# Optimization experiments

Hardware: AMD Instinct MI355X
Metric: run time of the kernel (lower is better)

Reference implementation:

```python
import jax, jax.numpy as jnp
import numpy as np

N_TOKENS = 16384
D_IN = 1024
D_HID = 4096
D_OUT = 1024
N_EXPERTS = 8


def setup_inputs() -> dict:
    key = jax.random.key(0)
    ks = jax.random.split(key, 7)
    s_in = 1.0 / np.sqrt(D_IN)
    s_hid = 1.0 / np.sqrt(D_HID)
    return {
        "x": jax.random.normal(ks[0], (N_TOKENS, D_IN), dtype=jnp.float32),
        "Wr": jax.random.uniform(ks[1], (D_IN, N_EXPERTS), jnp.float32, -s_in, s_in),
        "br": jax.random.uniform(ks[2], (N_EXPERTS,), jnp.float32, -s_in, s_in),
        "W1": jax.random.uniform(ks[3], (N_EXPERTS, D_IN, D_HID), jnp.float32, -s_in, s_in),
        "b1": jax.random.uniform(ks[4], (N_EXPERTS, D_HID), jnp.float32, -s_in, s_in),
        "W2": jax.random.uniform(ks[5], (N_EXPERTS, D_HID, D_OUT), jnp.float32, -s_hid, s_hid),
        "b2": jax.random.uniform(ks[6], (N_EXPERTS, D_OUT), jnp.float32, -s_hid, s_hid),
    }


def reference(x, Wr, br, W1, b1, W2, b2):
    # Router: softmax over expert logits, hard top-1 dispatch (argmax).
    # Note: output is NOT scaled by routing probs in the original module.
    logits = x @ Wr + br                      # [N, E]
    expert_idx = jnp.argmax(logits, axis=-1)  # [N] (argmax of softmax == argmax of logits)

    n_experts = W1.shape[0]
    out = jnp.zeros((x.shape[0], W2.shape[-1]), dtype=x.dtype)
    # world_size=1 -> all_to_all is identity; masked per-expert dense FFN + combine.
    # Fixed small loop over experts (structurally distinct weights), vectorized over tokens.
    for e in range(n_experts):
        mask = (expert_idx == e)[:, None]                 # [N, 1]
        xe = jnp.where(mask, x, 0.0)                      # zero out tokens not routed here
        y = jax.nn.relu(xe @ W1[e] + b1[e]) @ W2[e] + b2[e]  # [N, D_OUT]
        out = jnp.where(mask, y, out)
    return out
```

## Files before the change

kernel.cpp:

```cpp
#include <hip/hip_runtime.h>
#include <cstdint>

#define NT   16384
#define DIN  1024
#define DHID 4096
#define DOUT 1024
#define NE   8
#define NMT  136
#define NMT2 72

typedef unsigned short u16;
typedef short bf16x8 __attribute__((ext_vector_type(8)));
typedef float f32x4  __attribute__((ext_vector_type(4)));

__device__ __forceinline__ u16 f2b(float f) {
  union { float f; unsigned u; } a; a.f = f;
  unsigned u = a.u;
  return (u16)((u + 0x7FFFu + ((u >> 16) & 1u)) >> 16);
}

__device__ __forceinline__ void gl_lds16(const u16* g, u16* l) {
  __builtin_amdgcn_global_load_lds(
      (const __attribute__((address_space(1))) void*)g,
      (__attribute__((address_space(3))) void*)l,
      16, 0, 0);
}

__device__ __forceinline__ void barrier_raw() {
  asm volatile("" ::: "memory");
  __builtin_amdgcn_s_barrier();
  asm volatile("" ::: "memory");
}
__device__ __forceinline__ void lgkm0() {
  asm volatile("s_waitcnt lgkmcnt(0)" ::: "memory");
  __builtin_amdgcn_sched_barrier(0);
}
__device__ __forceinline__ void vm6() {
  asm volatile("s_waitcnt vmcnt(6)" ::: "memory");
}

__global__ void router_kernel(const float* __restrict__ x, const float* __restrict__ Wr,
                              const float* __restrict__ br, u16* __restrict__ Xb,
                              int* __restrict__ eidx, int* __restrict__ counts) {
  int t = blockIdx.x * 4 + (threadIdx.x >> 6);
  int lane = threadIdx.x & 63;
  const float4* xr = (const float4*)(x + (size_t)t * DIN);
  ushort4* xbr = (ushort4*)(Xb + (size_t)t * DIN);
  float acc[NE];
#pragma unroll
  for (int e = 0; e < NE; e++) acc[e] = 0.f;
#pragma unroll
  for (int i = 0; i < DIN / 256; i++) {
    int q = lane + i * 64;
    float4 xv = xr[q];
    ushort4 o;
    o.x = f2b(xv.x); o.y = f2b(xv.y); o.z = f2b(xv.z); o.w = f2b(xv.w);
    xbr[q] = o;
    const float* wp = Wr + (size_t)q * 4 * NE;
#pragma unroll
    for (int kk = 0; kk < 4; kk++) {
      float xs = (&xv.x)[kk];
      const float4 w0 = *(const float4*)(wp + kk * NE);
      const float4 w1 = *(const float4*)(wp + kk * NE + 4);
      acc[0] += xs * w0.x; acc[1] += xs * w0.y; acc[2] += xs * w0.z; acc[3] += xs * w0.w;
      acc[4] += xs * w1.x; acc[5] += xs * w1.y; acc[6] += xs * w1.z; acc[7] += xs * w1.w;
    }
  }
#pragma unroll
  for (int off = 32; off > 0; off >>= 1) {
#pragma unroll
    for (int e = 0; e < NE; e++) acc[e] += __shfl_down(acc[e], off, 64);
  }
  if (lane == 0) {
    int best = 0; float bv = acc[0] + br[0];
#pragma unroll
    for (int e = 1; e < NE; e++) {
      float v = acc[e] + br[e];
      if (v > bv) { bv = v; best = e; }
    }
    eidx[t] = best;
    atomicAdd(&counts[best], 1);
  }
}

__global__ void zero_kernel(int* __restrict__ p) {
  if (threadIdx.x < 16) p[threadIdx.x] = 0;
}

__global__ void scan_kernel(const int* __restrict__ counts, int* __restrict__ offsets,
                            int4* __restrict__ tiles, int4* __restrict__ tiles2) {
  if (threadIdx.x == 0) {
    int s = 0, nt = 0, nt2 = 0;
    for (int e = 0; e < NE; e++) {
      int c = counts[e];
      offsets[e] = s;
      for (int m0 = 0; m0 < c; m0 += 128) {
        int v = c - m0; if (v > 128) v = 128;
        tiles[nt++] = make_int4(e, s + m0, v, 0);
      }
      for (int m0 = 0; m0 < c; m0 += 256) {
        int v = c - m0; if (v > 256) v = 256;
        tiles2[nt2++] = make_int4(e, s + m0, v, 0);
      }
      s += c;
    }
    offsets[NE] = s;
    while (nt < NMT) tiles[nt++] = make_int4(0, 0, 0, 0);
    while (nt2 < NMT2) tiles2[nt2++] = make_int4(0, 0, 0, 0);
  }
}

__global__ void scatter_kernel(const int* __restrict__ eidx, const int* __restrict__ offsets,
                               int* __restrict__ cursor, int* __restrict__ perm) {
  int t = blockIdx.x * blockDim.x + threadIdx.x;
  if (t >= NT) return;
  int e = eidx[t];
  int pos = offsets[e] + atomicAdd(&cursor[e], 1);
  perm[pos] = t;
}

__global__ void transpose_cvt_all(const float* __restrict__ W1, const float* __restrict__ W2,
                                  u16* __restrict__ W1t, u16* __restrict__ W2t) {
  __shared__ float tile[64][65];
  int bid = blockIdx.x;
  const float* src; u16* dst; int K, H, k0, h0;
  if (bid < NE * 16 * 64) {
    int e = bid >> 10, rem = bid & 1023;
    K = DIN; H = DHID;
    k0 = (rem & 15) * 64; h0 = (rem >> 4) * 64;
    src = W1 + (size_t)e * DIN * DHID; dst = W1t + (size_t)e * DIN * DHID;
  } else {
    bid -= NE * 16 * 64;
    int e = bid >> 10, rem = bid & 1023;
    K = DHID; H = DOUT;
    k0 = (rem >> 4) * 64; h0 = (rem & 15) * 64;
    src = W2 + (size_t)e * DHID * DOUT; dst = W2t + (size_t)e * DHID * DOUT;
  }
  const int tid = threadIdx.x;
#pragma unroll
  for (int i = 0; i < 4; i++) {
    int idx = tid + i * 256;
    int r = idx >> 4;
    int c = (idx & 15) * 4;
    const float4 v = *(const float4*)(src + (size_t)(k0 + r) * H + h0 + c);
    tile[r][c] = v.x; tile[r][c + 1] = v.y; tile[r][c + 2] = v.z; tile[r][c + 3] = v.w;
  }
  __syncthreads();
#pragma unroll
  for (int i = 0; i < 4; i++) {
    int idx = tid + i * 256;
    int r = idx >> 4;
    int c = (idx & 15) * 4;
    ushort4 o;
    o.x = f2b(tile[c][r]); o.y = f2b(tile[c + 1][r]);
    o.z = f2b(tile[c + 2][r]); o.w = f2b(tile[c + 3][r]);
    *(ushort4*)(dst + (size_t)(h0 + r) * K + k0 + c) = o;
  }
}

template<bool GATHER_A, bool STORE_HIDDEN>
__global__ __launch_bounds__(256) void moe_gemm(
    const u16* __restrict__ A, const u16* __restrict__ Bt,
    const float* __restrict__ bias,
    const int* __restrict__ perm, const int4* __restrict__ tiles,
    u16* __restrict__ Hout, float* __restrict__ Fout,
    int K, int N) {
  const int4 ti = tiles[blockIdx.y];
  const int valid = ti.z;
  if (valid == 0) return;
  const int e = ti.x;
  const int base_p = ti.y;
  const int n0 = blockIdx.x * 128;

  __shared__ u16 sA[2 * 128 * 32];
  __shared__ u16 sB[2 * 128 * 32];

  const int tid = threadIdx.x;
  const int lane = tid & 63;
  const int wave = tid >> 6;
  const int wm = (wave >> 1) * 64;
  const int wn = (wave & 1) * 64;
  const int quad = lane >> 4;
  const int l15 = lane & 15;

  const int rr = lane >> 2;
  const int cb = (lane & 3) * 8;

  const int rA0 = wave * 16 + rr;
  const int rA1 = rA0 + 64;

  int pa0 = base_p + rA0; if (pa0 > NT - 1) pa0 = NT - 1;
  int pa1 = base_p + rA1; if (pa1 > NT - 1) pa1 = NT - 1;
  const int arow0 = GATHER_A ? perm[pa0] : pa0;
  const int arow1 = GATHER_A ? perm[pa1] : pa1;
  const u16* aptr0 = A + (size_t)arow0 * K + cb;
  const u16* aptr1 = A + (size_t)arow1 * K + cb;
  const u16* bptr0 = Bt + ((size_t)e * N + n0 + rA0) * K + cb;
  const u16* bptr1 = Bt + ((size_t)e * N + n0 + rA1) * K + cb;

  u16* dA0 = &sA[wave * 512];
  u16* dA1 = &sA[wave * 512 + 2048];
  u16* dB0 = &sB[wave * 512];
  u16* dB1 = &sB[wave * 512 + 2048];

  f32x4 acc[4][4];
#pragma unroll
  for (int mi = 0; mi < 4; mi++)
#pragma unroll
    for (int ni = 0; ni < 4; ni++)
      acc[mi][ni] = (f32x4){0.f, 0.f, 0.f, 0.f};

  const int kiters = K >> 6;
  for (int kt = 0; kt < kiters; kt++) {
    if (kt) __syncthreads();
    gl_lds16(aptr0,      dA0);
    gl_lds16(aptr1,      dA1);
    gl_lds16(bptr0,      dB0);
    gl_lds16(bptr1,      dB1);
    gl_lds16(aptr0 + 32, dA0 + 4096);
    gl_lds16(aptr1 + 32, dA1 + 4096);
    gl_lds16(bptr0 + 32, dB0 + 4096);
    gl_lds16(bptr1 + 32, dB1 + 4096);
    aptr0 += 64; aptr1 += 64; bptr0 += 64; bptr1 += 64;
    __syncthreads();

#pragma unroll
    for (int h = 0; h < 2; h++) {
      bf16x8 af[4], bfr[4];
#pragma unroll
      for (int mi = 0; mi < 4; mi++)
        af[mi] = *(const bf16x8*)&sA[h * 4096 + (wm + mi * 16 + l15) * 32 + quad * 8];
#pragma unroll
      for (int ni = 0; ni < 4; ni++)
        bfr[ni] = *(const bf16x8*)&sB[h * 4096 + (wn + ni * 16 + l15) * 32 + quad * 8];
#pragma unroll
      for (int mi = 0; mi < 4; mi++)
#pragma unroll
        for (int ni = 0; ni < 4; ni++)
          acc[mi][ni] = __builtin_amdgcn_mfma_f32_16x16x32_bf16(af[mi], bfr[ni], acc[mi][ni], 0, 0, 0);
    }
  }

  float bv[4];
#pragma unroll
  for (int ni = 0; ni < 4; ni++)
    bv[ni] = bias[(size_t)e * N + n0 + wn + ni * 16 + l15];

#pragma unroll
  for (int mi = 0; mi < 4; mi++) {
#pragma unroll
    for (int r = 0; r < 4; r++) {
      const int ml = wm + mi * 16 + quad * 4 + r;
      if (ml >= valid) continue;
      const int pp = base_p + ml;
      if (STORE_HIDDEN) {
        u16* orow = Hout + (size_t)pp * N + n0 + wn;
#pragma unroll
        for (int ni = 0; ni < 4; ni++) {
          float v = acc[mi][ni][r] + bv[ni];
          v = v > 0.f ? v : 0.f;
          orow[ni * 16 + l15] = f2b(v);
        }
      } else {
        const int token = perm[pp];
        float* orow = Fout + (size_t)token * N + n0 + wn;
#pragma unroll
        for (int ni = 0; ni < 4; ni++)
          orow[ni * 16 + l15] = acc[mi][ni][r] + bv[ni];
      }
    }
  }
}

#define RXA0 0
#define RXA1 8192
#define RXB0 16384
#define RXB1 24576
#define RYA0 32768
#define RYA1 40960
#define RYB0 49152
#define RYB1 57344

__global__ __launch_bounds__(512, 2) void moe_gemm1_8ph(
    const u16* __restrict__ A, const u16* __restrict__ Bt,
    const float* __restrict__ bias, const int* __restrict__ perm,
    const int4* __restrict__ tiles, u16* __restrict__ Hout) {
  const int4 ti = tiles[blockIdx.y];
  const int valid = ti.z;
  if (valid == 0) return;
  const int e = ti.x;
  const int base_p = ti.y;
  const int n0 = blockIdx.x * 256;

  __shared__ u16 lds[65536];

  const int tid = threadIdx.x;
  const int lane = tid & 63;
  const int w = tid >> 6;
  const int wr = w >> 2;
  const int wc = w & 3;
  const int quad = lane >> 4;
  const int l15 = lane & 15;

  const int srow = tid >> 3;
  const int klog = ((tid & 7) << 3) ^ ((srow & 7) << 3);
  int p0 = base_p + srow;        if (p0 > NT - 1) p0 = NT - 1;
  int p1 = base_p + 64 + srow;   if (p1 > NT - 1) p1 = NT - 1;
  int p2 = base_p + 128 + srow;  if (p2 > NT - 1) p2 = NT - 1;
  int p3 = base_p + 192 + srow;  if (p3 > NT - 1) p3 = NT - 1;
  const u16* pA00 = A + (size_t)perm[p0] * DIN + klog;
  const u16* pA01 = A + (size_t)perm[p1] * DIN + klog;
  const u16* pA10 = A + (size_t)perm[p2] * DIN + klog;
  const u16* pA11 = A + (size_t)perm[p3] * DIN + klog;
  const u16* pB00 = Bt + ((size_t)e * DHID + n0 + srow)       * DIN + klog;
  const u16* pB01 = Bt + ((size_t)e * DHID + n0 + 64 + srow)  * DIN + klog;
  const u16* pB10 = Bt + ((size_t)e * DHID + n0 + 128 + srow) * DIN + klog;
  const u16* pB11 = Bt + ((size_t)e * DHID + n0 + 192 + srow) * DIN + klog;

#define STG(RB, P0, P1, KO) \
  do { gl_lds16((P0) + (KO), &lds[(RB) + w * 512]); \
       gl_lds16((P1) + (KO), &lds[(RB) + 4096 + w * 512]); } while (0)

  STG(RXA0, pA00, pA01, 0);
  STG(RXA1, pA10, pA11, 0);
  STG(RXB0, pB00, pB01, 0);
  STG(RXB1, pB10, pB11, 0);
  STG(RYB0, pB00, pB01, 64);
  STG(RYB1, pB10, pB11, 64);
  STG(RYA0, pA00, pA01, 64);
  vm6();
  barrier_raw();

  const int aX = RXA0 + wr * 8192;
  const int bX = RXB0 + (wc >> 1) * 8192;
  const int aY = RYA0 + wr * 8192;
  const int bY = RYB0 + (wc >> 1) * 8192;
  const int swz = (l15 & 7) << 3;
  const int brow = (wc & 1) * 64 + l15;

  bf16x8 aF[4][2], bF[4][2];
  f32x4 acc[8][4];
#pragma unroll
  for (int i = 0; i < 8; i++)
#pragma unroll
    for (int j2 = 0; j2 < 4; j2++) acc[i][j2] = (f32x4){0.f, 0.f, 0.f, 0.f};

#define RDA(BASE, MH) do { _Pragma("unroll") \
  for (int mi = 0; mi < 4; mi++) { _Pragma("unroll") \
    for (int h = 0; h < 2; h++) \
      aF[mi][h] = *(const bf16x8*)&lds[(BASE) + ((MH) * 64 + mi * 16 + l15) * 64 + \
                                       ((h * 32 + quad * 8) ^ swz)]; } } while (0)

#define RDB(BASE) do { _Pragma("unroll") \
  for (int ni = 0; ni < 4; ni++) { _Pragma("unroll") \
    for (int h = 0; h < 2; h++) \
      bF[ni][h] = *(const bf16x8*)&lds[(BASE) + (brow + ni * 16) * 64 + \
                                       ((h * 32 + quad * 8) ^ swz)]; } } while (0)

#define MM(MH, NB) do { __builtin_amdgcn_s_setprio(1); _Pragma("unroll") \
  for (int mi = 0; mi < 4; mi++) { _Pragma("unroll") \
    for (int ni = 0; ni < 2; ni++) { _Pragma("unroll") \
      for (int h = 0; h < 2; h++) \
        acc[(MH) * 4 + mi][(NB) + ni] = __builtin_amdgcn_mfma_f32_16x16x32_bf16( \
            aF[mi][h], bF[(NB) + ni][h], acc[(MH) * 4 + mi][(NB) + ni], 0, 0, 0); } } \
  __builtin_amdgcn_s_setprio(0); } while (0)

  const int NITER = DIN / 128;
  for (int j = 0; j < NITER; j++) {
    const int ky1 = (2 * j + 1) * 64;
    int t2 = 2 * j + 2; if (t2 > 15) t2 = 15;
    int t3 = 2 * j + 3; if (t3 > 15) t3 = 15;
    const int kx = t2 * 64, ky2 = t3 * 64;
    RDA(aX, 0); RDB(bX);
    STG(RYA1, pA10, pA11, ky1);
    barrier_raw(); lgkm0();
    MM(0, 0);
    barrier_raw();
    STG(RXB0, pB00, pB01, kx);
    barrier_raw(); lgkm0();
    MM(0, 2);
    barrier_raw();
    RDA(aX, 1);
    STG(RXB1, pB10, pB11, kx);
    barrier_raw(); lgkm0();
    MM(1, 2);
    barrier_raw();
    STG(RXA0, pA00, pA01, kx);
    barrier_raw(); lgkm0();
    MM(1, 0);
    vm6();
    barrier_raw();
    RDA(aY, 0); RDB(bY);
    STG(RXA1, pA10, pA11, kx);
    barrier_raw(); lgkm0();
    MM(0, 0);
    barrier_raw();
    STG(RYB0, pB00, pB01, ky2);
    barrier_raw(); lgkm0();
    MM(0, 2);
    barrier_raw();
    RDA(aY, 1);
    STG(RYB1, pB10, pB11, ky2);
    barrier_raw(); lgkm0();
    MM(1, 2);
    barrier_raw();
    STG(RYA0, pA00, pA01, ky2);
    barrier_raw(); lgkm0();
    MM(1, 0);
    vm6();
    barrier_raw();
  }

  const int col0 = n0 + wc * 64;
  float bv[4];
#pragma unroll
  for (int ni = 0; ni < 4; ni++)
    bv[ni] = bias[(size_t)e * DHID + col0 + ni * 16 + l15];
#pragma unroll
  for (int mi8 = 0; mi8 < 8; mi8++) {
#pragma unroll
    for (int r = 0; r < 4; r++) {
      const int ml = wr * 128 + mi8 * 16 + quad * 4 + r;
      if (ml >= valid) continue;
      u16* orow = Hout + (size_t)(base_p + ml) * DHID + col0;
#pragma unroll
      for (int ni = 0; ni < 4; ni++) {
        float v = acc[mi8][ni][r] + bv[ni];
        v = v > 0.f ? v : 0.f;
        orow[ni * 16 + l15] = f2b(v);
      }
    }
  }
#undef STG
#undef RDA
#undef RDB
#undef MM
}

__global__ void sentinel_kernel(float* __restrict__ out, int n) {
  int i = blockIdx.x * blockDim.x + threadIdx.x;
  if (i < n) out[i] = 31337.0f;
}

extern "C" void kernel_launch(void* const* d_in, const int* in_sizes, int n_in,
                              void* d_out, int out_size, void* d_ws, size_t ws_size,
                              hipStream_t stream) {
  const float* x  = (const float*)d_in[0];
  const float* Wr = (const float*)d_in[1];
  const float* br = (const float*)d_in[2];
  const float* W1 = (const float*)d_in[3];
  const float* b1 = (const float*)d_in[4];
  const float* W2 = (const float*)d_in[5];
  const float* b2 = (const float*)d_in[6];
  float* out = (float*)d_out;

  const size_t szXb  = (size_t)NT * DIN * 2;
  const size_t szW1t = (size_t)NE * DIN * DHID * 2;
  const size_t szW2t = (size_t)NE * DHID * DOUT * 2;
  const size_t szHid = (size_t)NT * DHID * 2;
  char* ws = (char*)d_ws;
  u16* Xb   = (u16*)ws;
  u16* W1t  = (u16*)(ws + szXb);
  u16* W2t  = (u16*)(ws + szXb + szW1t);
  u16* Hid  = (u16*)(ws + szXb + szW1t + szW2t);
  int* perm = (int*)(ws + szXb + szW1t + szW2t + szHid);
  int* eidx = perm + NT;
  int* ctrl = eidx + NT;
  int* counts  = ctrl;
  int* cursor  = ctrl + 8;
  int* offsets = ctrl + 16;
  int4* tiles   = (int4*)(ctrl + 32);
  int4* tiles2  = tiles + NMT;
  const size_t NEED = szXb + szW1t + szW2t + szHid + (size_t)NT * 4 * 2 + 4096;

  if (ws_size < NEED) {
    sentinel_kernel<<<(out_size + 255) / 256, 256, 0, stream>>>(out, out_size);
    return;
  }

  zero_kernel<<<1, 64, 0, stream>>>(ctrl);
  transpose_cvt_all<<<NE * 16 * 64 * 2, 256, 0, stream>>>(W1, W2, W1t, W2t);
  router_kernel<<<NT / 4, 256, 0, stream>>>(x, Wr, br, Xb, eidx, counts);
  scan_kernel<<<1, 64, 0, stream>>>(counts, offsets, tiles, tiles2);
  scatter_kernel<<<NT / 256, 256, 0, stream>>>(eidx, offsets, cursor, perm);

  moe_gemm1_8ph<<<dim3(DHID / 256, NMT2), 512, 0, stream>>>(
      Xb, W1t, b1, perm, tiles2, Hid);
  moe_gemm<false, false><<<dim3(DOUT / 128, NMT), 256, 0, stream>>>(
      Hid, W2t, b2, perm, tiles, nullptr, out, DHID, DOUT);
}
```

Baseline: 1.016 ms.

## Remap MoE GEMM grids to 1D swizzled order and skip MFMA for empty wave rows

Both grouped GEMMs now use a 1D grid whose block index is remapped so that consecutive blocks cover different tiles across groups (g*17+j, g*9+j), spreading expert tiles across XCDs for better L2 reuse. Waves whose row range lies entirely beyond the valid row count of a partially filled tile skip LDS fragment reads and MFMA work, but still take part in staging and barriers. In the first GEMM the B-fragment read is also split into two halves so the second half is loaded just before it is used, which lowers register pressure. The cost is extra branching around the MFMA blocks and a fixed coupling of the remap to NMT/NMT2 sizes.

After: 991.2 us. 1.03x faster.

```diff
diff --git a/kernel.cpp b/kernel.cpp
--- a/kernel.cpp
+++ b/kernel.cpp
@@ -158,19 +158,24 @@
   }
 }
 
-template<bool GATHER_A, bool STORE_HIDDEN>
-__global__ __launch_bounds__(256) void moe_gemm(
+__global__ __launch_bounds__(256) void moe_gemm2(
     const u16* __restrict__ A, const u16* __restrict__ Bt,
     const float* __restrict__ bias,
     const int* __restrict__ perm, const int4* __restrict__ tiles,
-    u16* __restrict__ Hout, float* __restrict__ Fout,
-    int K, int N) {
-  const int4 ti = tiles[blockIdx.y];
+    float* __restrict__ Fout) {
+  const int bid = blockIdx.x;
+  const int g = bid & 7;
+  const int r_ = bid >> 3;
+  const int n = r_ & 7;
+  const int j = r_ >> 3;
+  const int m = g * 17 + j;
+  const int4 ti = tiles[m];
   const int valid = ti.z;
   if (valid == 0) return;
   const int e = ti.x;
   const int base_p = ti.y;
-  const int n0 = blockIdx.x * 128;
+  const int n0 = n * 128;
+  const int K = DHID, N = DOUT;
 
   __shared__ u16 sA[2 * 128 * 32];
   __shared__ u16 sB[2 * 128 * 32];
@@ -182,6 +187,7 @@
   const int wn = (wave & 1) * 64;
   const int quad = lane >> 4;
   const int l15 = lane & 15;
+  const bool alive = (wm < valid);
 
   const int rr = lane >> 2;
   const int cb = (lane & 3) * 8;
@@ -191,10 +197,8 @@
 
   int pa0 = base_p + rA0; if (pa0 > NT - 1) pa0 = NT - 1;
   int pa1 = base_p + rA1; if (pa1 > NT - 1) pa1 = NT - 1;
-  const int arow0 = GATHER_A ? perm[pa0] : pa0;
-  const int arow1 = GATHER_A ? perm[pa1] : pa1;
-  const u16* aptr0 = A + (size_t)arow0 * K + cb;
-  const u16* aptr1 = A + (size_t)arow1 * K + cb;
+  const u16* aptr0 = A + (size_t)pa0 * K + cb;
+  const u16* aptr1 = A + (size_t)pa1 * K + cb;
   const u16* bptr0 = Bt + ((size_t)e * N + n0 + rA0) * K + cb;
   const u16* bptr1 = Bt + ((size_t)e * N + n0 + rA1) * K + cb;
 
@@ -224,22 +228,25 @@
     aptr0 += 64; aptr1 += 64; bptr0 += 64; bptr1 += 64;
     __syncthreads();
 
-#pragma unroll
-    for (int h = 0; h < 2; h++) {
-      bf16x8 af[4], bfr[4];
-#pragma unroll
-      for (int mi = 0; mi < 4; mi++)
-        af[mi] = *(const bf16x8*)&sA[h * 4096 + (wm + mi * 16 + l15) * 32 + quad * 8];
-#pragma unroll
-      for (int ni = 0; ni < 4; ni++)
-        bfr[ni] = *(const bf16x8*)&sB[h * 4096 + (wn + ni * 16 + l15) * 32 + quad * 8];
-#pragma unroll
-      for (int mi = 0; mi < 4; mi++)
+    if (alive) {
+#pragma unroll
+      for (int h = 0; h < 2; h++) {
+        bf16x8 af[4], bfr[4];
+#pragma unroll
+        for (int mi = 0; mi < 4; mi++)
+          af[mi] = *(const bf16x8*)&sA[h * 4096 + (wm + mi * 16 + l15) * 32 + quad * 8];
 #pragma unroll
         for (int ni = 0; ni < 4; ni++)
-          acc[mi][ni] = __builtin_amdgcn_mfma_f32_16x16x32_bf16(af[mi], bfr[ni], acc[mi][ni], 0, 0, 0);
-    }
-  }
+          bfr[ni] = *(const bf16x8*)&sB[h * 4096 + (wn + ni * 16 + l15) * 32 + quad * 8];
+#pragma unroll
+        for (int mi = 0; mi < 4; mi++)
+#pragma unroll
+          for (int ni = 0; ni < 4; ni++)
+            acc[mi][ni] = __builtin_amdgcn_mfma_f32_16x16x32_bf16(af[mi], bfr[ni], acc[mi][ni], 0, 0, 0);
+      }
+    }
+  }
+  if (!alive) return;
 
   float bv[4];
 #pragma unroll
@@ -252,22 +259,11 @@
     for (int r = 0; r < 4; r++) {
       const int ml = wm + mi * 16 + quad * 4 + r;
       if (ml >= valid) continue;
-      const int pp = base_p + ml;
-      if (STORE_HIDDEN) {
-        u16* orow = Hout + (size_t)pp * N + n0 + wn;
-#pragma unroll
-        for (int ni = 0; ni < 4; ni++) {
-          float v = acc[mi][ni][r] + bv[ni];
-          v = v > 0.f ? v : 0.f;
-          orow[ni * 16 + l15] = f2b(v);
-        }
-      } else {
-        const int token = perm[pp];
-        float* orow = Fout + (size_t)token * N + n0 + wn;
-#pragma unroll
-        for (int ni = 0; ni < 4; ni++)
-          orow[ni * 16 + l15] = acc[mi][ni][r] + bv[ni];
-      }
+      const int token = perm[base_p + ml];
+      float* orow = Fout + (size_t)token * N + n0 + wn;
+#pragma unroll
+      for (int ni = 0; ni < 4; ni++)
+        orow[ni * 16 + l15] = acc[mi][ni][r] + bv[ni];
     }
   }
 }
@@ -285,12 +281,18 @@
     const u16* __restrict__ A, const u16* __restrict__ Bt,
     const float* __restrict__ bias, const int* __restrict__ perm,
     const int4* __restrict__ tiles, u16* __restrict__ Hout) {
-  const int4 ti = tiles[blockIdx.y];
+  const int bid = blockIdx.x;
+  const int g = bid & 7;
+  const int r_ = bid >> 3;
+  const int n = r_ & 15;
+  const int j_ = r_ >> 4;
+  const int m = g * 9 + j_;
+  const int4 ti = tiles[m];
   const int valid = ti.z;
   if (valid == 0) return;
   const int e = ti.x;
   const int base_p = ti.y;
-  const int n0 = blockIdx.x * 256;
+  const int n0 = n * 256;
 
   __shared__ u16 lds[65536];
 
@@ -301,6 +303,8 @@
   const int wc = w & 3;
   const int quad = lane >> 4;
   const int l15 = lane & 15;
+  const bool aliveLo = (valid > wr * 128);
+  const bool aliveHi = (valid > wr * 128 + 64);
 
   const int srow = tid >> 3;
   const int klog = ((tid & 7) << 3) ^ ((srow & 7) << 3);
@@ -345,25 +349,26 @@
 #pragma unroll
     for (int j2 = 0; j2 < 4; j2++) acc[i][j2] = (f32x4){0.f, 0.f, 0.f, 0.f};
 
-#define RDA(BASE, MH) do { _Pragma("unroll") \
+#define RDA(BASE, MH) do { if ((MH) ? aliveHi : aliveLo) { _Pragma("unroll") \
   for (int mi = 0; mi < 4; mi++) { _Pragma("unroll") \
     for (int h = 0; h < 2; h++) \
       aF[mi][h] = *(const bf16x8*)&lds[(BASE) + ((MH) * 64 + mi * 16 + l15) * 64 + \
-                                       ((h * 32 + quad * 8) ^ swz)]; } } while (0)
-
-#define RDB(BASE) do { _Pragma("unroll") \
-  for (int ni = 0; ni < 4; ni++) { _Pragma("unroll") \
+                                       ((h * 32 + quad * 8) ^ swz)]; } } } while (0)
+
+#define RDB2(BASE, NB) do { if (aliveLo) { _Pragma("unroll") \
+  for (int ni = 0; ni < 2; ni++) { _Pragma("unroll") \
     for (int h = 0; h < 2; h++) \
-      bF[ni][h] = *(const bf16x8*)&lds[(BASE) + (brow + ni * 16) * 64 + \
-                                       ((h * 32 + quad * 8) ^ swz)]; } } while (0)
-
-#define MM(MH, NB) do { __builtin_amdgcn_s_setprio(1); _Pragma("unroll") \
+      bF[(NB) + ni][h] = *(const bf16x8*)&lds[(BASE) + (brow + ((NB) + ni) * 16) * 64 + \
+                                              ((h * 32 + quad * 8) ^ swz)]; } } } while (0)
+
+#define MM(MH, NB) do { if ((MH) ? aliveHi : aliveLo) { \
+  __builtin_amdgcn_s_setprio(1); _Pragma("unroll") \
   for (int mi = 0; mi < 4; mi++) { _Pragma("unroll") \
     for (int ni = 0; ni < 2; ni++) { _Pragma("unroll") \
       for (int h = 0; h < 2; h++) \
         acc[(MH) * 4 + mi][(NB) + ni] = __builtin_amdgcn_mfma_f32_16x16x32_bf16( \
             aF[mi][h], bF[(NB) + ni][h], acc[(MH) * 4 + mi][(NB) + ni], 0, 0, 0); } } \
-  __builtin_amdgcn_s_setprio(0); } while (0)
+  __builtin_amdgcn_s_setprio(0); } } while (0)
 
   const int NITER = DIN / 128;
   for (int j = 0; j < NITER; j++) {
@@ -371,11 +376,12 @@
     int t2 = 2 * j + 2; if (t2 > 15) t2 = 15;
     int t3 = 2 * j + 3; if (t3 > 15) t3 = 15;
     const int kx = t2 * 64, ky2 = t3 * 64;
-    RDA(aX, 0); RDB(bX);
+    RDA(aX, 0); RDB2(bX, 0);
     STG(RYA1, pA10, pA11, ky1);
     barrier_raw(); lgkm0();
     MM(0, 0);
     barrier_raw();
+    RDB2(bX, 2);
     STG(RXB0, pB00, pB01, kx);
     barrier_raw(); lgkm0();
     MM(0, 2);
@@ -390,11 +396,12 @@
     MM(1, 0);
     vm6();
     barrier_raw();
-    RDA(aY, 0); RDB(bY);
+    RDA(aY, 0); RDB2(bY, 0);
     STG(RXA1, pA10, pA11, kx);
     barrier_raw(); lgkm0();
     MM(0, 0);
     barrier_raw();
+    RDB2(bY, 2);
     STG(RYB0, pB00, pB01, ky2);
     barrier_raw(); lgkm0();
     MM(0, 2);
@@ -433,7 +440,7 @@
   }
 #undef STG
 #undef RDA
-#undef RDB
+#undef RDB2
 #undef MM
 }
 
@@ -484,8 +491,6 @@
   scan_kernel<<<1, 64, 0, stream>>>(counts, offsets, tiles, tiles2);
   scatter_kernel<<<NT / 256, 256, 0, stream>>>(eidx, offsets, cursor, perm);
 
-  moe_gemm1_8ph<<<dim3(DHID / 256, NMT2), 512, 0, stream>>>(
-      Xb, W1t, b1, perm, tiles2, Hid);
-  moe_gemm<false, false><<<dim3(DOUT / 128, NMT), 256, 0, stream>>>(
-      Hid, W2t, b2, perm, tiles, nullptr, out, DHID, DOUT);
-}
+  moe_gemm1_8ph<<<16 * NMT2, 512, 0, stream>>>(Xb, W1t, b1, perm, tiles2, Hid);
+  moe_gemm2<<<8 * NMT, 256, 0, stream>>>(Hid, W2t, b2, perm, tiles, out);
+}
```
